# Kernel tuning notes

Measured on AMD Instinct MI355X. Metric: run time of the kernel, lower is better.

## Reference

```python
import jax, jax.numpy as jnp
import numpy as np

VOCAB, NUM_LABELS, EMB, H = 50000, 5, 512, 1024
B, S = 32, 256


def setup_inputs() -> dict:
    key = jax.random.key(0)
    ks = jax.random.split(key, 7)
    tokens = jax.random.randint(ks[0], (B, S), 0, VOCAB)
    scale_e = 0.05
    emb = jax.random.normal(ks[1], (VOCAB, EMB), dtype=jnp.float32) * scale_e
    # Keras LSTM kernels: input kernel [EMB,4H], recurrent kernel [H,4H], bias [4H]
    W = jax.random.normal(ks[2], (EMB, 4 * H), dtype=jnp.float32) / np.sqrt(EMB)
    U = jax.random.normal(ks[3], (H, 4 * H), dtype=jnp.float32) / np.sqrt(H)
    # unit_forget_bias=True: forget-gate bias block initialized to 1
    b = jnp.concatenate([
        jnp.zeros((H,), jnp.float32),
        jnp.ones((H,), jnp.float32),
        jnp.zeros((2 * H,), jnp.float32),
    ])
    Wd = jax.random.normal(ks[4], (H, NUM_LABELS), dtype=jnp.float32) / np.sqrt(H)
    bd = jnp.zeros((NUM_LABELS,), jnp.float32)
    return {"tokens": tokens, "emb": emb, "W": W, "U": U, "b": b, "Wd": Wd, "bd": bd}


def _lstm_last_h(x, W, U, b):
    # x: [B,S,EMB] -> last hidden state [B,H]
    xt = jnp.swapaxes(x, 0, 1)  # [S,B,EMB]
    # precompute input projections for all steps: [S,B,4H]
    xz = jnp.einsum('sbe,eg->sbg', xt, W) + b
    h0 = jnp.zeros((x.shape[0], H), x.dtype)
    c0 = jnp.zeros((x.shape[0], H), x.dtype)

    def step(carry, xz_t):
        h, c = carry
        z = xz_t + h @ U  # [B,4H]
        i, f, g, o = jnp.split(z, 4, axis=-1)  # Keras gate order i,f,c,o
        i = jax.nn.sigmoid(i)
        f = jax.nn.sigmoid(f)
        g = jnp.tanh(g)
        o = jax.nn.sigmoid(o)
        c = f * c + i * g
        h = o * jnp.tanh(c)
        return (h, c), None

    (h_last, _), _ = jax.lax.scan(step, (h0, c0), xz)
    return h_last


def reference(tokens, emb, W, U, b, Wd, bd):
    x = emb[tokens]  # [B,S,EMB] embedding lookup
    h = _lstm_last_h(x, W, U, b)  # [B,H]
    logits = h @ Wd + bd  # [B,NUM_LABELS]
    return logits
```

## Files before the change

kernel.cpp:

```cpp
#include <hip/hip_runtime.h>
#include <hip/hip_fp16.h>

#define B_   32
#define S_   256
#define EMB_ 512
#define H_   1024
#define G4_  4096
#define NL_  5
#define NBLK 128

typedef _Float16 f16x8 __attribute__((ext_vector_type(8)));
typedef float f32x4 __attribute__((ext_vector_type(4)));
typedef unsigned long long ull;

__device__ inline ull ldq(const ull* p) {
  return __hip_atomic_load(p, __ATOMIC_RELAXED, __HIP_MEMORY_SCOPE_AGENT);
}
__device__ inline void stw(unsigned* p, unsigned v) {
  __hip_atomic_store(p, v, __ATOMIC_RELAXED, __HIP_MEMORY_SCOPE_AGENT);
}

__global__ __launch_bounds__(256) void k_transposeK(const float* __restrict__ src,
                                                    float* __restrict__ dst, int K) {
  __shared__ float tile[32][33];
  int c0 = blockIdx.x * 32, k0 = blockIdx.y * 32;
  int tx = threadIdx.x & 31, ty = threadIdx.x >> 5;
#pragma unroll
  for (int i = 0; i < 4; ++i)
    tile[ty + 8 * i][tx] = src[(size_t)(k0 + ty + 8 * i) * G4_ + c0 + tx];
  __syncthreads();
#pragma unroll
  for (int i = 0; i < 4; ++i)
    dst[(size_t)(c0 + ty + 8 * i) * K + k0 + tx] = tile[tx][ty + 8 * i];
}

__global__ __launch_bounds__(256) void k_prepU16(const float* __restrict__ Ut,
                                                 f16x8* __restrict__ Ubf) {
  int gid = blockIdx.x * 256 + threadIdx.x;
  int l = gid & 63;
  int bxws = gid >> 6;
  int n = l & 15, kgrp = l >> 4;
  int s = bxws & 7, bw = bxws >> 3;
  int w = bw & 3, bx = bw >> 2;
  int g = n & 3, ju = n >> 2;
  int gcol = g * 1024 + bx * 4 + ju;
  int kbase = w * 256 + s * 32 + kgrp * 8;
  const float4* f = (const float4*)(Ut + (size_t)gcol * H_ + kbase);
  float4 f0 = f[0], f1 = f[1];
  float v[8] = {f0.x, f0.y, f0.z, f0.w, f1.x, f1.y, f1.z, f1.w};
  f16x8 vh, vl;
#pragma unroll
  for (int j = 0; j < 8; ++j) {
    _Float16 hi = (_Float16)v[j];
    vh[j] = hi;
    vl[j] = (_Float16)((v[j] - (float)hi) * 1024.f);
  }
  Ubf[(size_t)bxws * 128 + l] = vh;
  Ubf[(size_t)bxws * 128 + 64 + l] = vl;
}

__global__ __launch_bounds__(256) void k_prepW16(const float* __restrict__ Wt,
                                                 unsigned short* __restrict__ Wf16) {
  int gid = blockIdx.x * 256 + threadIdx.x;
  int l = gid & 63, fi = gid >> 6;
  int kc = fi & 15, ug = fi >> 4;
  int n16 = l & 15, kgrp = l >> 4;
  int gcol = (n16 & 3) * 1024 + ug * 4 + (n16 >> 2);
  const float4* f = (const float4*)(Wt + (size_t)gcol * 512 + kc * 32 + kgrp * 8);
  float4 f0 = f[0], f1 = f[1];
  float v[8] = {f0.x, f0.y, f0.z, f0.w, f1.x, f1.y, f1.z, f1.w};
  union { unsigned short u[8]; uint4 q; } o;
#pragma unroll
  for (int j = 0; j < 8; ++j) o.u[j] = __half_as_ushort(__float2half_rn(v[j]));
  *(uint4*)(Wf16 + ((size_t)fi * 64 + l) * 8) = o.q;
}

__global__ __launch_bounds__(256) void k_prepX(const int* __restrict__ tokens,
                                               const float* __restrict__ emb,
                                               unsigned short* __restrict__ Xf16) {
  int gid = blockIdx.x * 256 + threadIdx.x;
  int seg = gid & 63, row = gid >> 6;
  int s = row >> 5, b = row & 31;
  int tok = tokens[b * 256 + s];
  const float4* f = (const float4*)(emb + (size_t)tok * EMB_ + seg * 8);
  float4 f0 = f[0], f1 = f[1];
  float v[8] = {f0.x, f0.y, f0.z, f0.w, f1.x, f1.y, f1.z, f1.w};
  union { unsigned short u[8]; uint4 q; } o;
#pragma unroll
  for (int j = 0; j < 8; ++j) o.u[j] = __half_as_ushort(__float2half_rn(v[j]));
  *(uint4*)(Xf16 + (size_t)row * 512 + seg * 8) = o.q;
}

__global__ __launch_bounds__(512, 2) void k_steps9(
    const f16x8* __restrict__ Ubf,
    const unsigned short* __restrict__ Wf16,
    const unsigned short* __restrict__ Xf16,
    const float* __restrict__ bias,
    unsigned* __restrict__ T0, unsigned* __restrict__ T1,
    unsigned* __restrict__ flg) {
  __shared__ f16x8 UL[8192];
  __shared__ float red[4096];
  __shared__ float zg[1056];
  __shared__ float bias_s[32];

  const int tid = threadIdx.x;
  const int bx = blockIdx.x;
  const int l = tid & 63, w = tid >> 6;

#pragma unroll
  for (int i = 0; i < 16; ++i) {
    int flat = i * 512 + tid;
    int ll = flat & 63, s8 = (flat >> 6) & 7, ks = (flat >> 9) & 3;
    int pl = (flat >> 11) & 1, cg = flat >> 12;
    size_t fi = (size_t)((bx * 2 + cg) * 4 + ks) * 8 + s8;
    UL[flat] = Ubf[fi * 128 + pl * 64 + ll];
  }
  if (tid < 32) {
    int cg = tid >> 4, n16 = tid & 15;
    bias_s[tid] = bias[(n16 & 3) * 1024 + (bx * 2 + cg) * 4 + (n16 >> 2)];
  }

  const int e = tid & 255, m = tid >> 8;
  const int n16r = (e >> 2) & 15;
  const int zb = m * 16 + (e >> 6) * 4 + (e & 3);

  const int gb = tid & 31, gu = tid >> 5;
  const int widx = (((gb >> 4) * 128 + bx) * 16 + (gb & 15)) * 4 + (gu >> 1);
  const int zrd = gb * 33 + (gu >> 2) * 16 + (gu & 3) * 4;
  float creg = 0.f;

  const int ks_w = w >> 1;
  const int xrow0 = (l & 15) * 512 + (l >> 4) * 8;
  const unsigned* myflg = flg + (w * 16 + (l & 15)) * 32;

  __syncthreads();

  for (int t = 0; t < S_; ++t) {
    const ull* R64 = (const ull*)((t & 1) ? T0 : T1);
    unsigned* WrT = (t & 1) ? T1 : T0;

    f32x4 acc[2][2], accL[2][2];
#pragma unroll
    for (int cg = 0; cg < 2; ++cg)
#pragma unroll
      for (int m2 = 0; m2 < 2; ++m2) {
        acc[cg][m2] = (f32x4){0.f, 0.f, 0.f, 0.f};
        accL[cg][m2] = (f32x4){0.f, 0.f, 0.f, 0.f};
      }
    {
      const unsigned short* Xt = Xf16 + (size_t)t * 16384;
#pragma unroll
      for (int c2 = 0; c2 < 2; ++c2) {
        int kc = w * 2 + c2;
        f16x8 xa0 = *(const f16x8*)(Xt + xrow0 + kc * 32);
        f16x8 xa1 = *(const f16x8*)(Xt + 8192 + xrow0 + kc * 32);
        f16x8 wb0 = *(const f16x8*)(Wf16 + ((size_t)((bx * 2 + 0) * 16 + kc) * 64 + l) * 8);
        f16x8 wb1 = *(const f16x8*)(Wf16 + ((size_t)((bx * 2 + 1) * 16 + kc) * 64 + l) * 8);
        acc[0][0] = __builtin_amdgcn_mfma_f32_16x16x32_f16(xa0, wb0, acc[0][0], 0, 0, 0);
        acc[0][1] = __builtin_amdgcn_mfma_f32_16x16x32_f16(xa1, wb0, acc[0][1], 0, 0, 0);
        acc[1][0] = __builtin_amdgcn_mfma_f32_16x16x32_f16(xa0, wb1, acc[1][0], 0, 0, 0);
        acc[1][1] = __builtin_amdgcn_mfma_f32_16x16x32_f16(xa1, wb1, acc[1][1], 0, 0, 0);
      }
    }

    if (t > 0) {
      while (true) {
        unsigned v = __hip_atomic_load(myflg, __ATOMIC_RELAXED, __HIP_MEMORY_SCOPE_AGENT);
        if (__all((int)(v >= (unsigned)t))) break;
        __builtin_amdgcn_s_sleep(1);
      }
      union F { ull q[2]; f16x8 v; };
      F A[2][4];
#pragma unroll
      for (int m2 = 0; m2 < 2; ++m2)
#pragma unroll
        for (int s = 0; s < 4; ++s) {
          int kidx = w * 16 + s * 4 + (l >> 4);
          int b64 = ((m2 * 128 + kidx) * 16 + (l & 15)) * 2;
          A[m2][s].q[0] = ldq(R64 + b64);
          A[m2][s].q[1] = ldq(R64 + b64 + 1);
        }
#pragma unroll
      for (int s = 0; s < 4; ++s) {
        int s8 = (w & 1) * 4 + s;
#pragma unroll
        for (int cg = 0; cg < 2; ++cg) {
          f16x8 uhf = UL[cg * 4096 + ks_w * 512 + s8 * 64 + l];
          f16x8 ulf = UL[cg * 4096 + 2048 + ks_w * 512 + s8 * 64 + l];
          acc[cg][0]  = __builtin_amdgcn_mfma_f32_16x16x32_f16(A[0][s].v, uhf, acc[cg][0], 0, 0, 0);
          acc[cg][1]  = __builtin_amdgcn_mfma_f32_16x16x32_f16(A[1][s].v, uhf, acc[cg][1], 0, 0, 0);
          accL[cg][0] = __builtin_amdgcn_mfma_f32_16x16x32_f16(A[0][s].v, ulf, accL[cg][0], 0, 0, 0);
          accL[cg][1] = __builtin_amdgcn_mfma_f32_16x16x32_f16(A[1][s].v, ulf, accL[cg][1], 0, 0, 0);
        }
      }
    }

#pragma unroll
    for (int cg = 0; cg < 2; ++cg)
#pragma unroll
      for (int m2 = 0; m2 < 2; ++m2)
        acc[cg][m2] += accL[cg][m2] * 9.765625e-4f;

    if (w < 4) {
#pragma unroll
      for (int cg = 0; cg < 2; ++cg) {
        *(f32x4*)(&red[((w * 2 + 0) * 2 + cg) * 256 + l * 4]) = acc[cg][0];
        *(f32x4*)(&red[((w * 2 + 1) * 2 + cg) * 256 + l * 4]) = acc[cg][1];
      }
    }
    __syncthreads();
    if (w >= 4) {
      int w4 = w - 4;
#pragma unroll
      for (int cg = 0; cg < 2; ++cg) {
        f32x4* p0 = (f32x4*)(&red[((w4 * 2 + 0) * 2 + cg) * 256 + l * 4]);
        f32x4* p1 = (f32x4*)(&red[((w4 * 2 + 1) * 2 + cg) * 256 + l * 4]);
        *p0 += acc[cg][0];
        *p1 += acc[cg][1];
      }
    }
    __syncthreads();

    {
      float z0 = bias_s[n16r], z1 = bias_s[16 + n16r];
#pragma unroll
      for (int w4 = 0; w4 < 4; ++w4) {
        z0 += red[((w4 * 2 + m) * 2 + 0) * 256 + e];
        z1 += red[((w4 * 2 + m) * 2 + 1) * 256 + e];
      }
      zg[zb * 33 + n16r] = z0;
      zg[zb * 33 + 16 + n16r] = z1;
    }
    __syncthreads();

    if (tid < 256) {
      float zi = zg[zrd + 0];
      float zf = zg[zrd + 1];
      float zc_ = zg[zrd + 2];
      float zo = zg[zrd + 3];
      float ig = 1.f / (1.f + __expf(-zi));
      float fg = 1.f / (1.f + __expf(-zf));
      float gg = tanhf(zc_);
      float og = 1.f / (1.f + __expf(-zo));
      creg = fg * creg + ig * gg;
      float hv = og * tanhf(creg);
      unsigned pk = (unsigned)__half_as_ushort(__float2half_rn(hv));
      unsigned other = (unsigned)__shfl_xor((int)pk, 32, 64);
      if ((gu & 1) == 0)
        stw(WrT + widx, (pk & 0xffffu) | (other << 16));
    }
    __syncthreads();
    if (tid == 0)
      stw(flg + bx * 32, (unsigned)(t + 1));
  }
}

__global__ __launch_bounds__(256) void k_head6(const unsigned* __restrict__ T,
                                               const float* __restrict__ Wd,
                                               const float* __restrict__ bd,
                                               float* __restrict__ out) {
  __shared__ float red[32 * 9];
  int lbl = blockIdx.x;
  int tid = threadIdx.x;
  int b = tid >> 3, ks = tid & 7;
  float acc = 0.f;
  for (int k = ks * 128; k < ks * 128 + 128; ++k) {
    int idx = (((b >> 4) * 128 + (k >> 3)) * 16 + (b & 15)) * 4 + ((k & 7) >> 1);
    unsigned wv = T[idx];
    unsigned short h16 = (unsigned short)((k & 1) ? (wv >> 16) : (wv & 0xffffu));
    acc += __half2float(__ushort_as_half(h16)) * Wd[k * NL_ + lbl];
  }
  red[b * 9 + ks] = acc;
  __syncthreads();
  if (tid < 32) {
    float s = bd[lbl];
#pragma unroll
    for (int i = 0; i < 8; ++i) s += red[tid * 9 + i];
    out[tid * NL_ + lbl] = s;
  }
}

extern "C" void kernel_launch(void* const* d_in, const int* in_sizes, int n_in,
                              void* d_out, int out_size, void* d_ws, size_t ws_size,
                              hipStream_t stream) {
  const int* tokens  = (const int*)d_in[0];
  const float* emb   = (const float*)d_in[1];
  const float* W     = (const float*)d_in[2];
  const float* U     = (const float*)d_in[3];
  const float* bias  = (const float*)d_in[4];
  const float* Wd    = (const float*)d_in[5];
  const float* bd    = (const float*)d_in[6];
  float* out = (float*)d_out;

  char* ws = (char*)d_ws;
  unsigned short* Xf16 = (unsigned short*)ws;
  unsigned short* Wf16 = (unsigned short*)(ws + 8388608);
  float* Ut          = (float*)(ws + 16777216);
  float* Wt          = (float*)(ws + 33554432);
  f16x8* Ubf         = (f16x8*)(ws + 41943040);
  unsigned* T0       = (unsigned*)(ws + 50331648);
  unsigned* T1       = (unsigned*)(ws + 50397184);
  unsigned* flg      = (unsigned*)(ws + 50462720);

  hipMemsetAsync(flg, 0, 16384, stream);
  k_transposeK<<<dim3(128, 32), 256, 0, stream>>>(U, Ut, 1024);
  k_prepU16<<<2048, 256, 0, stream>>>(Ut, Ubf);
  k_transposeK<<<dim3(128, 16), 256, 0, stream>>>(W, Wt, 512);
  k_prepW16<<<1024, 256, 0, stream>>>(Wt, Wf16);
  k_prepX<<<2048, 256, 0, stream>>>(tokens, emb, Xf16);

  k_steps9<<<NBLK, 512, 0, stream>>>(Ubf, Wf16, Xf16, bias, T0, T1, flg);

  k_head6<<<NL_, 256, 0, stream>>>(T1, Wd, bd, out);
}
```

Baseline: 966.2 us.

## Split LSTM recurrence into 256 single-wave blocks with register-only gate math

The persistent recurrent kernel moves from 128 blocks of 512 threads to 256 blocks of one wavefront each, split by batch half and unit group. Each wave now computes the full K reduction itself, so the LDS reduction and the three block barriers per step are gone. Gate values are gathered with shuffles, and the sigmoid and tanh use fast reciprocal approximations. The trade-offs are a longer serial MFMA chain per wave, more flags to poll, and slightly lower activation accuracy.

```diff
diff --git a/kernel.cpp b/kernel.cpp
--- a/kernel.cpp
+++ b/kernel.cpp
@@ -7,7 +7,6 @@
 #define H_   1024
 #define G4_  4096
 #define NL_  5
-#define NBLK 128
 
 typedef _Float16 f16x8 __attribute__((ext_vector_type(8)));
 typedef float f32x4 __attribute__((ext_vector_type(4)));
@@ -16,8 +15,18 @@
 __device__ inline ull ldq(const ull* p) {
   return __hip_atomic_load(p, __ATOMIC_RELAXED, __HIP_MEMORY_SCOPE_AGENT);
 }
+__device__ inline unsigned ldw(const unsigned* p) {
+  return __hip_atomic_load(p, __ATOMIC_RELAXED, __HIP_MEMORY_SCOPE_AGENT);
+}
 __device__ inline void stw(unsigned* p, unsigned v) {
   __hip_atomic_store(p, v, __ATOMIC_RELAXED, __HIP_MEMORY_SCOPE_AGENT);
+}
+__device__ inline float sigm(float x) {
+  return __builtin_amdgcn_rcpf(1.f + __expf(-x));
+}
+__device__ inline float ftanh(float x) {
+  float e = __expf(2.f * x);
+  return (e - 1.f) * __builtin_amdgcn_rcpf(e + 1.f);
 }
 
 __global__ __launch_bounds__(256) void k_transposeK(const float* __restrict__ src,
@@ -91,7 +100,7 @@
   *(uint4*)(Xf16 + (size_t)row * 512 + seg * 8) = o.q;
 }
 
-__global__ __launch_bounds__(512, 2) void k_steps9(
+__global__ __launch_bounds__(64, 1) void k_steps10(
     const f16x8* __restrict__ Ubf,
     const unsigned short* __restrict__ Wf16,
     const unsigned short* __restrict__ Xf16,
@@ -99,159 +108,114 @@
     unsigned* __restrict__ T0, unsigned* __restrict__ T1,
     unsigned* __restrict__ flg) {
   __shared__ f16x8 UL[8192];
-  __shared__ float red[4096];
-  __shared__ float zg[1056];
-  __shared__ float bias_s[32];
-
-  const int tid = threadIdx.x;
+
+  const int l = threadIdx.x;
   const int bx = blockIdx.x;
-  const int l = tid & 63, w = tid >> 6;
-
-#pragma unroll
-  for (int i = 0; i < 16; ++i) {
-    int flat = i * 512 + tid;
-    int ll = flat & 63, s8 = (flat >> 6) & 7, ks = (flat >> 9) & 3;
-    int pl = (flat >> 11) & 1, cg = flat >> 12;
-    size_t fi = (size_t)((bx * 2 + cg) * 4 + ks) * 8 + s8;
-    UL[flat] = Ubf[fi * 128 + pl * 64 + ll];
-  }
-  if (tid < 32) {
-    int cg = tid >> 4, n16 = tid & 15;
-    bias_s[tid] = bias[(n16 & 3) * 1024 + (bx * 2 + cg) * 4 + (n16 >> 2)];
-  }
-
-  const int e = tid & 255, m = tid >> 8;
-  const int n16r = (e >> 2) & 15;
-  const int zb = m * 16 + (e >> 6) * 4 + (e & 3);
-
-  const int gb = tid & 31, gu = tid >> 5;
-  const int widx = (((gb >> 4) * 128 + bx) * 16 + (gb & 15)) * 4 + (gu >> 1);
-  const int zrd = gb * 33 + (gu >> 2) * 16 + (gu & 3) * 4;
-  float creg = 0.f;
-
-  const int ks_w = w >> 1;
-  const int xrow0 = (l & 15) * 512 + (l >> 4) * 8;
-  const unsigned* myflg = flg + (w * 16 + (l & 15)) * 32;
-
+  const int m = bx & 1;
+  const int ugp = bx >> 1;
+
+  for (int i = 0; i < 128; ++i) {
+    int ug2 = i >> 6, pl = (i >> 5) & 1, s = i & 31;
+    int ks = s >> 3, s8 = s & 7;
+    size_t fi = (size_t)((2 * ugp + ug2) * 4 + ks) * 8 + s8;
+    UL[i * 64 + l] = Ubf[fi * 128 + pl * 64 + l];
+  }
   __syncthreads();
+
+  const int g = l & 3, ju = (l & 15) >> 2, kg = l >> 4, row = l & 15;
+  float bia[2];
+#pragma unroll
+  for (int ug2 = 0; ug2 < 2; ++ug2)
+    bia[ug2] = bias[g * 1024 + (2 * ugp + ug2) * 4 + ju];
+  const int xbase = m * 8192 + row * 512 + kg * 8;
+  const unsigned stbase = (unsigned)((m * 128 + ugp) * 16) * 4;
+  float c_st[2][4] = {{0.f, 0.f, 0.f, 0.f}, {0.f, 0.f, 0.f, 0.f}};
+  const unsigned* FP = flg + (size_t)m * 128 * 16;
 
   for (int t = 0; t < S_; ++t) {
     const ull* R64 = (const ull*)((t & 1) ? T0 : T1);
     unsigned* WrT = (t & 1) ? T1 : T0;
 
-    f32x4 acc[2][2], accL[2][2];
-#pragma unroll
-    for (int cg = 0; cg < 2; ++cg)
-#pragma unroll
-      for (int m2 = 0; m2 < 2; ++m2) {
-        acc[cg][m2] = (f32x4){0.f, 0.f, 0.f, 0.f};
-        accL[cg][m2] = (f32x4){0.f, 0.f, 0.f, 0.f};
-      }
+    f32x4 accH[2], accL[2];
+#pragma unroll
+    for (int u2 = 0; u2 < 2; ++u2) {
+      accH[u2] = (f32x4){0.f, 0.f, 0.f, 0.f};
+      accL[u2] = (f32x4){0.f, 0.f, 0.f, 0.f};
+    }
+
     {
       const unsigned short* Xt = Xf16 + (size_t)t * 16384;
 #pragma unroll
-      for (int c2 = 0; c2 < 2; ++c2) {
-        int kc = w * 2 + c2;
-        f16x8 xa0 = *(const f16x8*)(Xt + xrow0 + kc * 32);
-        f16x8 xa1 = *(const f16x8*)(Xt + 8192 + xrow0 + kc * 32);
-        f16x8 wb0 = *(const f16x8*)(Wf16 + ((size_t)((bx * 2 + 0) * 16 + kc) * 64 + l) * 8);
-        f16x8 wb1 = *(const f16x8*)(Wf16 + ((size_t)((bx * 2 + 1) * 16 + kc) * 64 + l) * 8);
-        acc[0][0] = __builtin_amdgcn_mfma_f32_16x16x32_f16(xa0, wb0, acc[0][0], 0, 0, 0);
-        acc[0][1] = __builtin_amdgcn_mfma_f32_16x16x32_f16(xa1, wb0, acc[0][1], 0, 0, 0);
-        acc[1][0] = __builtin_amdgcn_mfma_f32_16x16x32_f16(xa0, wb1, acc[1][0], 0, 0, 0);
-        acc[1][1] = __builtin_amdgcn_mfma_f32_16x16x32_f16(xa1, wb1, acc[1][1], 0, 0, 0);
+      for (int kc = 0; kc < 16; ++kc) {
+        f16x8 xa = *(const f16x8*)(Xt + xbase + kc * 32);
+#pragma unroll
+        for (int ug2 = 0; ug2 < 2; ++ug2) {
+          f16x8 wb = *(const f16x8*)(Wf16 +
+              ((size_t)((2 * ugp + ug2) * 16 + kc) * 64 + l) * 8);
+          accH[ug2] = __builtin_amdgcn_mfma_f32_16x16x32_f16(xa, wb, accH[ug2], 0, 0, 0);
+        }
       }
     }
 
     if (t > 0) {
+      const unsigned tg = (unsigned)t;
       while (true) {
-        unsigned v = __hip_atomic_load(myflg, __ATOMIC_RELAXED, __HIP_MEMORY_SCOPE_AGENT);
-        if (__all((int)(v >= (unsigned)t))) break;
-        __builtin_amdgcn_s_sleep(1);
-      }
-      union F { ull q[2]; f16x8 v; };
-      F A[2][4];
-#pragma unroll
-      for (int m2 = 0; m2 < 2; ++m2)
-#pragma unroll
-        for (int s = 0; s < 4; ++s) {
-          int kidx = w * 16 + s * 4 + (l >> 4);
-          int b64 = ((m2 * 128 + kidx) * 16 + (l & 15)) * 2;
-          A[m2][s].q[0] = ldq(R64 + b64);
-          A[m2][s].q[1] = ldq(R64 + b64 + 1);
+        unsigned f0 = ldw(FP + l * 16);
+        unsigned f1 = ldw(FP + (64 + l) * 16);
+        if (__all((int)(f0 >= tg && f1 >= tg))) break;
+        __builtin_amdgcn_s_sleep(2);
+      }
+      ull A[32][2];
+#pragma unroll
+      for (int s = 0; s < 32; ++s) {
+        int kidx = s * 4 + kg;
+        int b64 = ((m * 128 + kidx) * 16 + row) * 2;
+        A[s][0] = ldq(R64 + b64);
+        A[s][1] = ldq(R64 + b64 + 1);
+      }
+#pragma unroll
+      for (int s = 0; s < 32; ++s) {
+        union { ull q[2]; f16x8 v; } a;
+        a.q[0] = A[s][0];
+        a.q[1] = A[s][1];
+#pragma unroll
+        for (int ug2 = 0; ug2 < 2; ++ug2) {
+          f16x8 uh = UL[(ug2 * 64 + s) * 64 + l];
+          f16x8 ulv = UL[(ug2 * 64 + 32 + s) * 64 + l];
+          accH[ug2] = __builtin_amdgcn_mfma_f32_16x16x32_f16(a.v, uh, accH[ug2], 0, 0, 0);
+          accL[ug2] = __builtin_amdgcn_mfma_f32_16x16x32_f16(a.v, ulv, accL[ug2], 0, 0, 0);
         }
-#pragma unroll
-      for (int s = 0; s < 4; ++s) {
-        int s8 = (w & 1) * 4 + s;
-#pragma unroll
-        for (int cg = 0; cg < 2; ++cg) {
-          f16x8 uhf = UL[cg * 4096 + ks_w * 512 + s8 * 64 + l];
-          f16x8 ulf = UL[cg * 4096 + 2048 + ks_w * 512 + s8 * 64 + l];
-          acc[cg][0]  = __builtin_amdgcn_mfma_f32_16x16x32_f16(A[0][s].v, uhf, acc[cg][0], 0, 0, 0);
-          acc[cg][1]  = __builtin_amdgcn_mfma_f32_16x16x32_f16(A[1][s].v, uhf, acc[cg][1], 0, 0, 0);
-          accL[cg][0] = __builtin_amdgcn_mfma_f32_16x16x32_f16(A[0][s].v, ulf, accL[cg][0], 0, 0, 0);
-          accL[cg][1] = __builtin_amdgcn_mfma_f32_16x16x32_f16(A[1][s].v, ulf, accL[cg][1], 0, 0, 0);
+      }
+    }
+
+#pragma unroll
+    for (int ug2 = 0; ug2 < 2; ++ug2) {
+#pragma unroll
+      for (int r = 0; r < 4; ++r) {
+        float zv = accH[ug2][r] + accL[ug2][r] * 9.765625e-4f + bia[ug2];
+        int base = l & ~3;
+        float zi = __shfl(zv, base);
+        float zf = __shfl(zv, base + 1);
+        float zc = __shfl(zv, base + 2);
+        float zo = __shfl(zv, base + 3);
+        float ig = sigm(zi);
+        float fg = sigm(zf);
+        float gg = ftanh(zc);
+        float og = sigm(zo);
+        float cn = fg * c_st[ug2][r] + ig * gg;
+        c_st[ug2][r] = cn;
+        float hv = og * ftanh(cn);
+        unsigned pk = (unsigned)__half_as_ushort(__float2half_rn(hv));
+        unsigned other = (unsigned)__shfl_xor((int)pk, 4, 64);
+        if ((l & 7) == 0) {
+          unsigned widx = stbase + ((unsigned)((l >> 4) * 4 + r)) * 4 +
+                          ug2 * 2 + (ju >> 1);
+          stw(WrT + widx, (pk & 0xffffu) | (other << 16));
         }
       }
     }
-
-#pragma unroll
-    for (int cg = 0; cg < 2; ++cg)
-#pragma unroll
-      for (int m2 = 0; m2 < 2; ++m2)
-        acc[cg][m2] += accL[cg][m2] * 9.765625e-4f;
-
-    if (w < 4) {
-#pragma unroll
-      for (int cg = 0; cg < 2; ++cg) {
-        *(f32x4*)(&red[((w * 2 + 0) * 2 + cg) * 256 + l * 4]) = acc[cg][0];
-        *(f32x4*)(&red[((w * 2 + 1) * 2 + cg) * 256 + l * 4]) = acc[cg][1];
-      }
-    }
-    __syncthreads();
-    if (w >= 4) {
-      int w4 = w - 4;
-#pragma unroll
-      for (int cg = 0; cg < 2; ++cg) {
-        f32x4* p0 = (f32x4*)(&red[((w4 * 2 + 0) * 2 + cg) * 256 + l * 4]);
-        f32x4* p1 = (f32x4*)(&red[((w4 * 2 + 1) * 2 + cg) * 256 + l * 4]);
-        *p0 += acc[cg][0];
-        *p1 += acc[cg][1];
-      }
-    }
-    __syncthreads();
-
-    {
-      float z0 = bias_s[n16r], z1 = bias_s[16 + n16r];
-#pragma unroll
-      for (int w4 = 0; w4 < 4; ++w4) {
-        z0 += red[((w4 * 2 + m) * 2 + 0) * 256 + e];
-        z1 += red[((w4 * 2 + m) * 2 + 1) * 256 + e];
-      }
-      zg[zb * 33 + n16r] = z0;
-      zg[zb * 33 + 16 + n16r] = z1;
-    }
-    __syncthreads();
-
-    if (tid < 256) {
-      float zi = zg[zrd + 0];
-      float zf = zg[zrd + 1];
-      float zc_ = zg[zrd + 2];
-      float zo = zg[zrd + 3];
-      float ig = 1.f / (1.f + __expf(-zi));
-      float fg = 1.f / (1.f + __expf(-zf));
-      float gg = tanhf(zc_);
-      float og = 1.f / (1.f + __expf(-zo));
-      creg = fg * creg + ig * gg;
-      float hv = og * tanhf(creg);
-      unsigned pk = (unsigned)__half_as_ushort(__float2half_rn(hv));
-      unsigned other = (unsigned)__shfl_xor((int)pk, 32, 64);
-      if ((gu & 1) == 0)
-        stw(WrT + widx, (pk & 0xffffu) | (other << 16));
-    }
-    __syncthreads();
-    if (tid == 0)
-      stw(flg + bx * 32, (unsigned)(t + 1));
+    asm volatile("s_waitcnt vmcnt(0)" ::: "memory");
+    if (l == 0) stw(flg + (size_t)(m * 128 + ugp) * 16, (unsigned)(t + 1));
   }
 }
 
@@ -298,9 +262,9 @@
   float* Ut          = (float*)(ws + 16777216);
   float* Wt          = (float*)(ws + 33554432);
   f16x8* Ubf         = (f16x8*)(ws + 41943040);
-  unsigned* T0       = (unsigned*)(ws + 50331648);
-  unsigned* T1       = (unsigned*)(ws + 50397184);
-  unsigned* flg      = (unsigned*)(ws + 50462720);
+  unsigned* T0       = (unsigned*)(ws + 58720256);
+  unsigned* T1       = (unsigned*)(ws + 58785792);
+  unsigned* flg      = (unsigned*)(ws + 58851328);
 
   hipMemsetAsync(flg, 0, 16384, stream);
   k_transposeK<<<dim3(128, 32), 256, 0, stream>>>(U, Ut, 1024);
@@ -309,7 +273,7 @@
   k_prepW16<<<1024, 256, 0, stream>>>(Wt, Wf16);
   k_prepX<<<2048, 256, 0, stream>>>(tokens, emb, Xf16);
 
-  k_steps9<<<NBLK, 512, 0, stream>>>(Ubf, Wf16, Xf16, bias, T0, T1, flg);
+  k_steps10<<<256, 64, 0, stream>>>(Ubf, Wf16, Xf16, bias, T0, T1, flg);
 
   k_head6<<<NL_, 256, 0, stream>>>(T1, Wd, bd, out);
 }
```

Result: slower. 2.304 ms (+138.5%).

## Fuse gate reduction into activation pass and publish per-wave step flags

Applied to the files above, without the earlier changes.

The partial-sum reduction and the gate activation now happen in one pass. Each of the first 256 threads reads its four gate pre-activations straight from the reduction buffer and keeps the bias in registers, which removes the zg staging buffer and one block barrier per timestep. Each of the four producing waves now publishes its own flag right after its h stores drain, instead of one thread publishing after a final barrier. Consumers poll the matching per-wave flag, which shortens the critical path of the recurrent cross-block handoff. The cost is 4x more flag slots to poll and more scattered LDS reads.

```diff
diff --git a/kernel.cpp b/kernel.cpp
--- a/kernel.cpp
+++ b/kernel.cpp
@@ -14,6 +14,9 @@
 typedef unsigned long long ull;
 
 __device__ inline ull ldq(const ull* p) {
+  return __hip_atomic_load(p, __ATOMIC_RELAXED, __HIP_MEMORY_SCOPE_AGENT);
+}
+__device__ inline unsigned ldw(const unsigned* p) {
   return __hip_atomic_load(p, __ATOMIC_RELAXED, __HIP_MEMORY_SCOPE_AGENT);
 }
 __device__ inline void stw(unsigned* p, unsigned v) {
@@ -91,7 +94,7 @@
   *(uint4*)(Xf16 + (size_t)row * 512 + seg * 8) = o.q;
 }
 
-__global__ __launch_bounds__(512, 2) void k_steps9(
+__global__ __launch_bounds__(512, 2) void k_steps11(
     const f16x8* __restrict__ Ubf,
     const unsigned short* __restrict__ Wf16,
     const unsigned short* __restrict__ Xf16,
@@ -100,8 +103,6 @@
     unsigned* __restrict__ flg) {
   __shared__ f16x8 UL[8192];
   __shared__ float red[4096];
-  __shared__ float zg[1056];
-  __shared__ float bias_s[32];
 
   const int tid = threadIdx.x;
   const int bx = blockIdx.x;
@@ -115,23 +116,20 @@
     size_t fi = (size_t)((bx * 2 + cg) * 4 + ks) * 8 + s8;
     UL[flat] = Ubf[fi * 128 + pl * 64 + ll];
   }
-  if (tid < 32) {
-    int cg = tid >> 4, n16 = tid & 15;
-    bias_s[tid] = bias[(n16 & 3) * 1024 + (bx * 2 + cg) * 4 + (n16 >> 2)];
-  }
-
-  const int e = tid & 255, m = tid >> 8;
-  const int n16r = (e >> 2) & 15;
-  const int zb = m * 16 + (e >> 6) * 4 + (e & 3);
 
   const int gb = tid & 31, gu = tid >> 5;
+  const int gm2 = gb >> 4, gcg = gu >> 2, gju = gu & 3;
+  const int gle = ((gb & 15) >> 2) * 16 + gju * 4;
+  const int grr = gb & 3;
   const int widx = (((gb >> 4) * 128 + bx) * 16 + (gb & 15)) * 4 + (gu >> 1);
-  const int zrd = gb * 33 + (gu >> 2) * 16 + (gu & 3) * 4;
+  float bia[4];
+#pragma unroll
+  for (int g = 0; g < 4; ++g) bia[g] = bias[g * 1024 + bx * 8 + gu];
   float creg = 0.f;
 
   const int ks_w = w >> 1;
   const int xrow0 = (l & 15) * 512 + (l >> 4) * 8;
-  const unsigned* myflg = flg + (w * 16 + (l & 15)) * 32;
+  const unsigned* myflg = flg + (size_t)((w * 16 + (l >> 2)) * 4 + (l & 3)) * 16;
 
   __syncthreads();
 
@@ -164,9 +162,10 @@
     }
 
     if (t > 0) {
+      const unsigned tg = (unsigned)t;
       while (true) {
-        unsigned v = __hip_atomic_load(myflg, __ATOMIC_RELAXED, __HIP_MEMORY_SCOPE_AGENT);
-        if (__all((int)(v >= (unsigned)t))) break;
+        unsigned v = ldw(myflg);
+        if (__all((int)(v >= tg))) break;
         __builtin_amdgcn_s_sleep(1);
       }
       union F { ull q[2]; f16x8 v; };
@@ -221,37 +220,32 @@
     }
     __syncthreads();
 
-    {
-      float z0 = bias_s[n16r], z1 = bias_s[16 + n16r];
+    if (tid < 256) {
+      float z[4];
+#pragma unroll
+      for (int g = 0; g < 4; ++g) z[g] = bia[g];
 #pragma unroll
       for (int w4 = 0; w4 < 4; ++w4) {
-        z0 += red[((w4 * 2 + m) * 2 + 0) * 256 + e];
-        z1 += red[((w4 * 2 + m) * 2 + 1) * 256 + e];
-      }
-      zg[zb * 33 + n16r] = z0;
-      zg[zb * 33 + 16 + n16r] = z1;
-    }
-    __syncthreads();
-
-    if (tid < 256) {
-      float zi = zg[zrd + 0];
-      float zf = zg[zrd + 1];
-      float zc_ = zg[zrd + 2];
-      float zo = zg[zrd + 3];
-      float ig = 1.f / (1.f + __expf(-zi));
-      float fg = 1.f / (1.f + __expf(-zf));
-      float gg = tanhf(zc_);
-      float og = 1.f / (1.f + __expf(-zo));
+        int sb = ((w4 * 2 + gm2) * 2 + gcg) * 256;
+#pragma unroll
+        for (int g = 0; g < 4; ++g)
+          z[g] += red[sb + (gle + g) * 4 + grr];
+      }
+      float ig = 1.f / (1.f + __expf(-z[0]));
+      float fg = 1.f / (1.f + __expf(-z[1]));
+      float gg = tanhf(z[2]);
+      float og = 1.f / (1.f + __expf(-z[3]));
       creg = fg * creg + ig * gg;
       float hv = og * tanhf(creg);
       unsigned pk = (unsigned)__half_as_ushort(__float2half_rn(hv));
       unsigned other = (unsigned)__shfl_xor((int)pk, 32, 64);
       if ((gu & 1) == 0)
         stw(WrT + widx, (pk & 0xffffu) | (other << 16));
+      asm volatile("s_waitcnt vmcnt(0)" ::: "memory");
+      if ((tid & 63) == 0)
+        stw(flg + (size_t)(bx * 4 + (tid >> 6)) * 16, (unsigned)(t + 1));
     }
     __syncthreads();
-    if (tid == 0)
-      stw(flg + bx * 32, (unsigned)(t + 1));
   }
 }
 
@@ -298,18 +292,18 @@
   float* Ut          = (float*)(ws + 16777216);
   float* Wt          = (float*)(ws + 33554432);
   f16x8* Ubf         = (f16x8*)(ws + 41943040);
-  unsigned* T0       = (unsigned*)(ws + 50331648);
-  unsigned* T1       = (unsigned*)(ws + 50397184);
-  unsigned* flg      = (unsigned*)(ws + 50462720);
-
-  hipMemsetAsync(flg, 0, 16384, stream);
+  unsigned* T0       = (unsigned*)(ws + 58720256);
+  unsigned* T1       = (unsigned*)(ws + 58785792);
+  unsigned* flg      = (unsigned*)(ws + 58851328);
+
+  hipMemsetAsync(flg, 0, 32768, stream);
   k_transposeK<<<dim3(128, 32), 256, 0, stream>>>(U, Ut, 1024);
   k_prepU16<<<2048, 256, 0, stream>>>(Ut, Ubf);
   k_transposeK<<<dim3(128, 16), 256, 0, stream>>>(W, Wt, 512);
   k_prepW16<<<1024, 256, 0, stream>>>(Wt, Wf16);
   k_prepX<<<2048, 256, 0, stream>>>(tokens, emb, Xf16);
 
-  k_steps9<<<NBLK, 512, 0, stream>>>(Ubf, Wf16, Xf16, bias, T0, T1, flg);
+  k_steps11<<<NBLK, 512, 0, stream>>>(Ubf, Wf16, Xf16, bias, T0, T1, flg);
 
   k_head6<<<NL_, 256, 0, stream>>>(T1, Wd, bd, out);
 }
```

Result: slower. 1.139 ms (+17.9%).
